# Optimization experiments

Measured on AMD Instinct MI355X. Metric: run time of the kernel, lower is better.

Reference implementation:

```python
import jax, jax.numpy as jnp
import numpy as np

N_NODES = 100000
N_EDGES = 1600000


def gcn_layer(x, src, dst, W, b, n_nodes):
    # PyG GCNConv: h = x @ W; add self-loops; sym-normalized scatter-add; + bias
    h = x @ W
    loop = jnp.arange(n_nodes, dtype=src.dtype)
    si = jnp.concatenate([src, loop])
    di = jnp.concatenate([dst, loop])
    deg = jax.ops.segment_sum(jnp.ones(si.shape[0], h.dtype), di, num_segments=n_nodes)
    dinv = jax.lax.rsqrt(deg)  # deg >= 1 due to self-loops
    norm = dinv[si] * dinv[di]              # [E+N]
    msgs = h[si] * norm[:, None]            # gather-scale
    out = jax.ops.segment_sum(msgs, di, num_segments=n_nodes)  # scatter-add
    return out + b


def setup_inputs() -> dict:
    key = jax.random.key(0)
    ks = jax.random.split(key, 8)
    x = jax.random.normal(ks[0], (N_NODES, 8), dtype=jnp.float32)
    edge_index = jax.random.randint(ks[1], (2, N_EDGES), 0, N_NODES, dtype=jnp.int32)
    W1 = jax.random.normal(ks[2], (8, 32), dtype=jnp.float32) * 0.3
    b1 = jax.random.normal(ks[3], (32,), dtype=jnp.float32) * 0.1
    W2 = jax.random.normal(ks[4], (32, 16), dtype=jnp.float32) * 0.2
    b2 = jax.random.normal(ks[5], (16,), dtype=jnp.float32) * 0.1
    Wfc = jax.random.normal(ks[6], (16, 1), dtype=jnp.float32) * 0.25
    bfc = jax.random.normal(ks[7], (1,), dtype=jnp.float32) * 0.1
    return {"x": x, "edge_index": edge_index, "W1": W1, "b1": b1,
            "W2": W2, "b2": b2, "Wfc": Wfc, "bfc": bfc}


def reference(x, edge_index, W1, b1, W2, b2, Wfc, bfc):
    n = x.shape[0]
    src, dst = edge_index[0], edge_index[1]
    h = jax.nn.relu(gcn_layer(x, src, dst, W1, b1, n))
    h = jax.nn.relu(gcn_layer(h, src, dst, W2, b2, n))
    return jax.nn.sigmoid(h @ Wfc + bfc)  # [N, 1]
```

## Files before the change

### kernel.cpp

```cpp
#include <hip/hip_runtime.h>
#include <math.h>

#define N_NODES 100000
#define N_EDGES 1600000

#define NB_SHIFT 7
#define NB 128
#define NBINS 782
#define RCAP 2432
#define BCHUNK 2048
#define BINBLOCKS ((N_EDGES + BCHUNK - 1) / BCHUNK)
#define LCAP 8
#define SPB 16

__device__ __forceinline__ unsigned int pack_bf2(float a, float b) {
    unsigned int ua = __float_as_uint(a), ub = __float_as_uint(b);
    ua += 0x7FFFu + ((ua >> 16) & 1u);
    ub += 0x7FFFu + ((ub >> 16) & 1u);
    return (ua >> 16) | (ub & 0xFFFF0000u);
}
__device__ __forceinline__ float bf_lo(unsigned int u) { return __uint_as_float(u << 16); }
__device__ __forceinline__ float bf_hi(unsigned int u) { return __uint_as_float(u & 0xFFFF0000u); }

#define QR(v) { v += __shfl_xor(v, 1, 64); v += __shfl_xor(v, 2, 64); }

__global__ __launch_bounds__(512) void k_bin(const int* __restrict__ src, const int* __restrict__ dst,
                                             unsigned char* __restrict__ cnt_tab, int* __restrict__ log,
                                             int* __restrict__ spill_rec, int* __restrict__ spill_bin, int e) {
    __shared__ int lcnt[NBINS];
    __shared__ int lbuf[NBINS * LCAP];
    __shared__ int sp_rec[SPB];
    __shared__ int sp_bin[SPB];
    __shared__ int sp_n;
    int tid = threadIdx.x, blk = blockIdx.x;
    for (int b = tid; b < NBINS; b += 512) lcnt[b] = 0;
    if (tid == 0) sp_n = 0;
    __syncthreads();
    int base = blk * BCHUNK;
    int end = min(base + BCHUNK, e);
    for (int i = base + tid; i < end; i += 512) {
        int d = dst[i], s = src[i];
        int b = d >> NB_SHIFT;
        int rec = (s << NB_SHIFT) | (d & (NB - 1));
        int slot = atomicAdd(&lcnt[b], 1);
        if (slot < LCAP) {
            lbuf[b * LCAP + slot] = rec;
        } else {
            int k = atomicAdd(&sp_n, 1);
            if (k < SPB) { sp_rec[k] = rec; sp_bin[k] = b; }
        }
    }
    __syncthreads();
    for (int b = tid; b < NBINS; b += 512) cnt_tab[blk * NBINS + b] = (unsigned char)min(lcnt[b], LCAP);
    int* lrow = log + blk * NBINS * LCAP;
    for (int idx = tid; idx < NBINS * LCAP; idx += 512) {
        int c = idx >> 3;
        if ((idx & (LCAP - 1)) < lcnt[c]) lrow[idx] = lbuf[idx];
    }
    if (tid < SPB) {
        int valid = tid < min(sp_n, SPB);
        spill_rec[blk * SPB + tid] = valid ? sp_rec[tid] : 0;
        spill_bin[blk * SPB + tid] = valid ? sp_bin[tid] : -1;
    }
}

__global__ __launch_bounds__(512) void k_sort(const unsigned char* __restrict__ cnt_tab, const int* __restrict__ log,
                                              const int* __restrict__ spill_rec, const int* __restrict__ spill_bin,
                                              int* __restrict__ gcur, int* __restrict__ regions,
                                              const float* __restrict__ x, float* __restrict__ dinv,
                                              unsigned int* __restrict__ gxu, int* __restrict__ row_start) {
    __shared__ int ccnt[BINBLOCKS];
    __shared__ int coff[BINBLOCKS];
    __shared__ int wtot[8];
    __shared__ int msum_s;
    __shared__ int sp_take;
    __shared__ int lrec[RCAP];
    __shared__ int lsort[RCAP];
    __shared__ int cnt[NB];
    __shared__ int stt[NB];
    __shared__ int cur[NB];
    __shared__ float di_s[NB];
    int b = blockIdx.x, tid = threadIdx.x;
    int lane = tid & 63, wv = tid >> 6;

    for (int c = tid; c < BINBLOCKS; c += 512) ccnt[c] = cnt_tab[c * NBINS + b];
    if (tid == 0) sp_take = 0;
    if (tid < NB) cnt[tid] = 0;
    __syncthreads();
    {
        int c0 = tid * 2, c1 = c0 + 1;
        int v0 = (c0 < BINBLOCKS) ? ccnt[c0] : 0;
        int v1 = (c1 < BINBLOCKS) ? ccnt[c1] : 0;
        int v = v0 + v1, sc = v;
#pragma unroll
        for (int off = 1; off < 64; off <<= 1) {
            int t = __shfl_up(sc, off, 64);
            if (lane >= off) sc += t;
        }
        if (lane == 63) wtot[wv] = sc;
        __syncthreads();
        if (tid == 0) {
            int acc = 0;
#pragma unroll
            for (int w = 0; w < 8; ++w) { int t = wtot[w]; wtot[w] = acc; acc += t; }
            msum_s = acc;
        }
        __syncthreads();
        int basep = sc - v + wtot[wv];
        if (c0 < BINBLOCKS) coff[c0] = basep;
        if (c1 < BINBLOCKS) coff[c1] = basep + v0;
    }
    __syncthreads();
    for (int idx = tid; idx < BINBLOCKS * LCAP; idx += 512) {
        int c = idx >> 3, k = idx & (LCAP - 1);
        if (k < ccnt[c]) {
            int pos = coff[c] + k;
            if (pos < RCAP) {
                int rec = log[(c * NBINS + b) * LCAP + k];
                lrec[pos] = rec;
                atomicAdd(&cnt[rec & (NB - 1)], 1);
            }
        }
    }
    for (int jj = tid; jj < BINBLOCKS * SPB; jj += 512) {
        if (spill_bin[jj] == b) {
            int p = atomicAdd(&sp_take, 1);
            int pos = msum_s + p;
            if (pos < RCAP) {
                int rec = spill_rec[jj];
                lrec[pos] = rec;
                atomicAdd(&cnt[rec & (NB - 1)], 1);
            }
        }
    }
    __syncthreads();
    int m = min(msum_s + sp_take, RCAP);
    if (tid == 0) gcur[b] = m;
    if (tid < 64) {
        int c0 = cnt[lane], c1 = cnt[64 + lane];
        int s0 = c0, s1 = c1;
#pragma unroll
        for (int off = 1; off < 64; off <<= 1) {
            int t0 = __shfl_up(s0, off, 64);
            int t1 = __shfl_up(s1, off, 64);
            if (lane >= off) { s0 += t0; s1 += t1; }
        }
        s1 += __shfl(s0, 63, 64);
        stt[lane] = s0 - c0;
        stt[64 + lane] = s1 - c1;
    }
    __syncthreads();
    int node0 = b << NB_SHIFT;
    if (tid < NB) {
        cur[tid] = stt[tid];
        float d = rsqrtf((float)cnt[tid] + 1.0f);
        di_s[tid] = d;
        row_start[b * NB + tid] = b * RCAP + stt[tid];
        int node = node0 + tid;
        if (node < N_NODES) dinv[node] = d;
    }
    __syncthreads();
    {
        int l = tid >> 2, p = tid & 3;
        int node = node0 + l;
        if (node < N_NODES) {
            const float2* x2 = (const float2*)x;
            float2 xv = x2[node * 4 + p];
            float d = di_s[l];
            gxu[node * 4 + p] = pack_bf2(xv.x * d, xv.y * d);
        }
    }
    for (int j = tid; j < m; j += 512) {
        int rec = lrec[j];
        int pos = atomicAdd(&cur[rec & (NB - 1)], 1);
        lsort[pos] = rec >> NB_SHIFT;
    }
    __syncthreads();
    int* wb = regions + b * RCAP;
    for (int j = tid; j < m; j += 512) wb[j] = lsort[j];
}

__global__ __launch_bounds__(512) void k_agg1_mlp(const int* __restrict__ gcur, const int* __restrict__ regions,
                                                  const int* __restrict__ row_start,
                                                  const unsigned int* __restrict__ gxu,
                                                  const float* __restrict__ dinv,
                                                  const float* __restrict__ W1, const float* __restrict__ b1,
                                                  const float* __restrict__ W2,
                                                  unsigned int* __restrict__ g2u) {
    __shared__ int lsort[RCAP];
    __shared__ float wsh[800];
    int b = blockIdx.x, tid = threadIdx.x;
    int m = gcur[b];
    const int* rrow = regions + b * RCAP;
    for (int j = tid; j < m; j += 512) lsort[j] = rrow[j];
    for (int i2 = tid; i2 < 800; i2 += 512)
        wsh[i2] = (i2 < 256) ? W1[i2] : (i2 < 288) ? b1[i2 - 256] : W2[i2 - 288];
    __syncthreads();
    int l = tid >> 2, q = tid & 3;
    int node = (b << NB_SHIFT) + l;
    if (node >= N_NODES) return;
    int js = row_start[node] - b * RCAP;
    int je = (l < NB - 1) ? (row_start[node + 1] - b * RCAP) : m;
    const uint4* gx4 = (const uint4*)gxu;
    float a0 = 0.f, a1 = 0.f, a2 = 0.f, a3 = 0.f, a4 = 0.f, a5 = 0.f, a6 = 0.f, a7 = 0.f;
    if (q == 0) {
        uint4 u = gx4[node];
        a0 = bf_lo(u.x); a1 = bf_hi(u.x); a2 = bf_lo(u.y); a3 = bf_hi(u.y);
        a4 = bf_lo(u.z); a5 = bf_hi(u.z); a6 = bf_lo(u.w); a7 = bf_hi(u.w);
    }
    int j = js + q;
    for (; j + 4 < je; j += 8) {
        int s0 = lsort[j], s1 = lsort[j + 4];
        uint4 u = gx4[s0];
        uint4 w = gx4[s1];
        a0 += bf_lo(u.x); a1 += bf_hi(u.x); a2 += bf_lo(u.y); a3 += bf_hi(u.y);
        a4 += bf_lo(u.z); a5 += bf_hi(u.z); a6 += bf_lo(u.w); a7 += bf_hi(u.w);
        a0 += bf_lo(w.x); a1 += bf_hi(w.x); a2 += bf_lo(w.y); a3 += bf_hi(w.y);
        a4 += bf_lo(w.z); a5 += bf_hi(w.z); a6 += bf_lo(w.w); a7 += bf_hi(w.w);
    }
    if (j < je) {
        uint4 u = gx4[lsort[j]];
        a0 += bf_lo(u.x); a1 += bf_hi(u.x); a2 += bf_lo(u.y); a3 += bf_hi(u.y);
        a4 += bf_lo(u.z); a5 += bf_hi(u.z); a6 += bf_lo(u.w); a7 += bf_hi(u.w);
    }
    QR(a0); QR(a1); QR(a2); QR(a3); QR(a4); QR(a5); QR(a6); QR(a7);
    float di = dinv[node];
    float y[8] = { a0 * di, a1 * di, a2 * di, a3 * di, a4 * di, a5 * di, a6 * di, a7 * di };
    const float* W1s = wsh;
    const float* b1s = wsh + 256;
    const float* W2s = wsh + 288;
    float hh[8];
#pragma unroll
    for (int ff = 0; ff < 8; ++ff) {
        int f = q * 8 + ff;
        float sa = b1s[f];
#pragma unroll
        for (int k = 0; k < 8; ++k) sa = fmaf(y[k], W1s[k * 32 + f], sa);
        hh[ff] = fmaxf(0.f, sa);
    }
    float g[16];
#pragma unroll
    for (int o = 0; o < 16; ++o) {
        float sa = 0.f;
#pragma unroll
        for (int ff = 0; ff < 8; ++ff) sa = fmaf(hh[ff], W2s[(q * 8 + ff) * 16 + o], sa);
        g[o] = sa;
    }
#pragma unroll
    for (int o = 0; o < 16; ++o) QR(g[o]);
    int f0 = q * 4;
    uint2 pk = make_uint2(pack_bf2(g[f0] * di, g[f0 + 1] * di),
                          pack_bf2(g[f0 + 2] * di, g[f0 + 3] * di));
    ((uint2*)g2u)[node * 4 + q] = pk;
}

__global__ __launch_bounds__(512) void k_agg2_final(const int* __restrict__ gcur, const int* __restrict__ regions,
                                                    const int* __restrict__ row_start,
                                                    const unsigned int* __restrict__ g2u,
                                                    const float* __restrict__ dinv,
                                                    const float* __restrict__ b2, const float* __restrict__ Wfc,
                                                    const float* __restrict__ bfc, float* __restrict__ out) {
    __shared__ int lsort[RCAP];
    int b = blockIdx.x, tid = threadIdx.x;
    int m = gcur[b];
    const int* rrow = regions + b * RCAP;
    for (int j = tid; j < m; j += 512) lsort[j] = rrow[j];
    __syncthreads();
    int l = tid >> 2, q = tid & 3;
    int node = (b << NB_SHIFT) + l;
    if (node >= N_NODES) return;
    int js = row_start[node] - b * RCAP;
    int je = (l < NB - 1) ? (row_start[node + 1] - b * RCAP) : m;
    const uint4* g24 = (const uint4*)g2u;
    float a[16];
#pragma unroll
    for (int f = 0; f < 16; ++f) a[f] = 0.f;
    if (q == 0) {
        uint4 u0 = g24[node * 2], u1 = g24[node * 2 + 1];
        a[0] = bf_lo(u0.x); a[1] = bf_hi(u0.x); a[2] = bf_lo(u0.y); a[3] = bf_hi(u0.y);
        a[4] = bf_lo(u0.z); a[5] = bf_hi(u0.z); a[6] = bf_lo(u0.w); a[7] = bf_hi(u0.w);
        a[8] = bf_lo(u1.x); a[9] = bf_hi(u1.x); a[10] = bf_lo(u1.y); a[11] = bf_hi(u1.y);
        a[12] = bf_lo(u1.z); a[13] = bf_hi(u1.z); a[14] = bf_lo(u1.w); a[15] = bf_hi(u1.w);
    }
    int j = js + q;
    for (; j + 4 < je; j += 8) {
        int s0 = lsort[j], s1 = lsort[j + 4];
        uint4 u0 = g24[s0 * 2], u1 = g24[s0 * 2 + 1];
        uint4 w0 = g24[s1 * 2], w1 = g24[s1 * 2 + 1];
        a[0] += bf_lo(u0.x); a[1] += bf_hi(u0.x); a[2] += bf_lo(u0.y); a[3] += bf_hi(u0.y);
        a[4] += bf_lo(u0.z); a[5] += bf_hi(u0.z); a[6] += bf_lo(u0.w); a[7] += bf_hi(u0.w);
        a[8] += bf_lo(u1.x); a[9] += bf_hi(u1.x); a[10] += bf_lo(u1.y); a[11] += bf_hi(u1.y);
        a[12] += bf_lo(u1.z); a[13] += bf_hi(u1.z); a[14] += bf_lo(u1.w); a[15] += bf_hi(u1.w);
        a[0] += bf_lo(w0.x); a[1] += bf_hi(w0.x); a[2] += bf_lo(w0.y); a[3] += bf_hi(w0.y);
        a[4] += bf_lo(w0.z); a[5] += bf_hi(w0.z); a[6] += bf_lo(w0.w); a[7] += bf_hi(w0.w);
        a[8] += bf_lo(w1.x); a[9] += bf_hi(w1.x); a[10] += bf_lo(w1.y); a[11] += bf_hi(w1.y);
        a[12] += bf_lo(w1.z); a[13] += bf_hi(w1.z); a[14] += bf_lo(w1.w); a[15] += bf_hi(w1.w);
    }
    if (j < je) {
        int s0 = lsort[j];
        uint4 u0 = g24[s0 * 2], u1 = g24[s0 * 2 + 1];
        a[0] += bf_lo(u0.x); a[1] += bf_hi(u0.x); a[2] += bf_lo(u0.y); a[3] += bf_hi(u0.y);
        a[4] += bf_lo(u0.z); a[5] += bf_hi(u0.z); a[6] += bf_lo(u0.w); a[7] += bf_hi(u0.w);
        a[8] += bf_lo(u1.x); a[9] += bf_hi(u1.x); a[10] += bf_lo(u1.y); a[11] += bf_hi(u1.y);
        a[12] += bf_lo(u1.z); a[13] += bf_hi(u1.z); a[14] += bf_lo(u1.w); a[15] += bf_hi(u1.w);
    }
#pragma unroll
    for (int f = 0; f < 16; ++f) QR(a[f]);
    if (q == 0) {
        float di = dinv[node];
        float z = bfc[0];
#pragma unroll
        for (int f = 0; f < 16; ++f)
            z += fmaxf(0.f, di * a[f] + b2[f]) * Wfc[f];
        out[node] = 1.0f / (1.0f + expf(-z));
    }
}

extern "C" void kernel_launch(void* const* d_in, const int* in_sizes, int n_in,
                              void* d_out, int out_size, void* d_ws, size_t ws_size,
                              hipStream_t stream) {
    const float* x   = (const float*)d_in[0];
    const int*   ei  = (const int*)d_in[1];
    const float* W1  = (const float*)d_in[2];
    const float* b1  = (const float*)d_in[3];
    const float* W2  = (const float*)d_in[4];
    const float* b2  = (const float*)d_in[5];
    const float* Wfc = (const float*)d_in[6];
    const float* bfc = (const float*)d_in[7];
    float* out = (float*)d_out;

    const int* src = ei;
    const int* dst = ei + N_EDGES;
    const int E = N_EDGES;

    int*           log       = (int*)d_ws;
    int*           spill_rec = log + (size_t)BINBLOCKS * NBINS * LCAP;
    int*           spill_bin = spill_rec + BINBLOCKS * SPB;
    int*           gcur      = spill_bin + BINBLOCKS * SPB;
    int*           regions   = gcur + NBINS;
    int*           row_start = regions + NBINS * RCAP;
    float*         dinv      = (float*)(row_start + NBINS * NB);
    unsigned int*  gxu       = (unsigned int*)(dinv + N_NODES);
    unsigned int*  g2u       = gxu + (size_t)N_NODES * 4;
    unsigned char* cnt_tab   = (unsigned char*)(g2u + (size_t)N_NODES * 8);

    k_bin<<<BINBLOCKS, 512, 0, stream>>>(src, dst, cnt_tab, log, spill_rec, spill_bin, E);
    k_sort<<<NBINS, 512, 0, stream>>>(cnt_tab, log, spill_rec, spill_bin, gcur, regions, x, dinv, gxu, row_start);
    k_agg1_mlp<<<NBINS, 512, 0, stream>>>(gcur, regions, row_start, gxu, dinv, W1, b1, W2, g2u);
    k_agg2_final<<<NBINS, 512, 0, stream>>>(gcur, regions, row_start, g2u, dinv, b2, Wfc, bfc, out);
}
```

Measured before the change: 144.7 us.

## Bin edges directly into global per-bin regions via atomic cursors

The binning kernel now reserves space in each bin's global region with one atomicAdd per (block, bin) and writes its local records straight there, with overflow records appended individually. This drops the intermediate log, count table and spill arrays, and with them the prefix scan and the per-chunk gather loop in the sort kernel, which now just reads its region. A memset of the bin counters is added. Record order within a bin becomes nondeterministic, and there are many scattered small global writes and contended atomics on about 782 counters.

```diff
diff --git a/kernel.cpp b/kernel.cpp
--- a/kernel.cpp
+++ b/kernel.cpp
@@ -11,7 +11,6 @@
 #define BCHUNK 2048
 #define BINBLOCKS ((N_EDGES + BCHUNK - 1) / BCHUNK)
 #define LCAP 8
-#define SPB 16
 
 __device__ __forceinline__ unsigned int pack_bf2(float a, float b) {
     unsigned int ua = __float_as_uint(a), ub = __float_as_uint(b);
@@ -25,16 +24,11 @@
 #define QR(v) { v += __shfl_xor(v, 1, 64); v += __shfl_xor(v, 2, 64); }
 
 __global__ __launch_bounds__(512) void k_bin(const int* __restrict__ src, const int* __restrict__ dst,
-                                             unsigned char* __restrict__ cnt_tab, int* __restrict__ log,
-                                             int* __restrict__ spill_rec, int* __restrict__ spill_bin, int e) {
+                                             int* __restrict__ gbin_cnt, int* __restrict__ regions, int e) {
     __shared__ int lcnt[NBINS];
     __shared__ int lbuf[NBINS * LCAP];
-    __shared__ int sp_rec[SPB];
-    __shared__ int sp_bin[SPB];
-    __shared__ int sp_n;
     int tid = threadIdx.x, blk = blockIdx.x;
     for (int b = tid; b < NBINS; b += 512) lcnt[b] = 0;
-    if (tid == 0) sp_n = 0;
     __syncthreads();
     int base = blk * BCHUNK;
     int end = min(base + BCHUNK, e);
@@ -46,34 +40,27 @@
         if (slot < LCAP) {
             lbuf[b * LCAP + slot] = rec;
         } else {
-            int k = atomicAdd(&sp_n, 1);
-            if (k < SPB) { sp_rec[k] = rec; sp_bin[k] = b; }
-        }
-    }
-    __syncthreads();
-    for (int b = tid; b < NBINS; b += 512) cnt_tab[blk * NBINS + b] = (unsigned char)min(lcnt[b], LCAP);
-    int* lrow = log + blk * NBINS * LCAP;
-    for (int idx = tid; idx < NBINS * LCAP; idx += 512) {
-        int c = idx >> 3;
-        if ((idx & (LCAP - 1)) < lcnt[c]) lrow[idx] = lbuf[idx];
-    }
-    if (tid < SPB) {
-        int valid = tid < min(sp_n, SPB);
-        spill_rec[blk * SPB + tid] = valid ? sp_rec[tid] : 0;
-        spill_bin[blk * SPB + tid] = valid ? sp_bin[tid] : -1;
-    }
-}
-
-__global__ __launch_bounds__(512) void k_sort(const unsigned char* __restrict__ cnt_tab, const int* __restrict__ log,
-                                              const int* __restrict__ spill_rec, const int* __restrict__ spill_bin,
-                                              int* __restrict__ gcur, int* __restrict__ regions,
+            int gp = atomicAdd(&gbin_cnt[b], 1);
+            if (gp < RCAP) regions[b * RCAP + gp] = rec;
+        }
+    }
+    __syncthreads();
+    for (int b = tid; b < NBINS; b += 512) {
+        int c = min(lcnt[b], LCAP);
+        if (c > 0) {
+            int gp = atomicAdd(&gbin_cnt[b], c);
+            int* row = regions + b * RCAP;
+#pragma unroll 4
+            for (int k = 0; k < c; ++k)
+                if (gp + k < RCAP) row[gp + k] = lbuf[b * LCAP + k];
+        }
+    }
+}
+
+__global__ __launch_bounds__(512) void k_sort(const int* __restrict__ gbin_cnt,
+                                              int* __restrict__ regions,
                                               const float* __restrict__ x, float* __restrict__ dinv,
                                               unsigned int* __restrict__ gxu, int* __restrict__ row_start) {
-    __shared__ int ccnt[BINBLOCKS];
-    __shared__ int coff[BINBLOCKS];
-    __shared__ int wtot[8];
-    __shared__ int msum_s;
-    __shared__ int sp_take;
     __shared__ int lrec[RCAP];
     __shared__ int lsort[RCAP];
     __shared__ int cnt[NB];
@@ -81,61 +68,17 @@
     __shared__ int cur[NB];
     __shared__ float di_s[NB];
     int b = blockIdx.x, tid = threadIdx.x;
-    int lane = tid & 63, wv = tid >> 6;
-
-    for (int c = tid; c < BINBLOCKS; c += 512) ccnt[c] = cnt_tab[c * NBINS + b];
-    if (tid == 0) sp_take = 0;
+    int lane = tid & 63;
+    int m = min(gbin_cnt[b], RCAP);
     if (tid < NB) cnt[tid] = 0;
     __syncthreads();
-    {
-        int c0 = tid * 2, c1 = c0 + 1;
-        int v0 = (c0 < BINBLOCKS) ? ccnt[c0] : 0;
-        int v1 = (c1 < BINBLOCKS) ? ccnt[c1] : 0;
-        int v = v0 + v1, sc = v;
-#pragma unroll
-        for (int off = 1; off < 64; off <<= 1) {
-            int t = __shfl_up(sc, off, 64);
-            if (lane >= off) sc += t;
-        }
-        if (lane == 63) wtot[wv] = sc;
-        __syncthreads();
-        if (tid == 0) {
-            int acc = 0;
-#pragma unroll
-            for (int w = 0; w < 8; ++w) { int t = wtot[w]; wtot[w] = acc; acc += t; }
-            msum_s = acc;
-        }
-        __syncthreads();
-        int basep = sc - v + wtot[wv];
-        if (c0 < BINBLOCKS) coff[c0] = basep;
-        if (c1 < BINBLOCKS) coff[c1] = basep + v0;
-    }
-    __syncthreads();
-    for (int idx = tid; idx < BINBLOCKS * LCAP; idx += 512) {
-        int c = idx >> 3, k = idx & (LCAP - 1);
-        if (k < ccnt[c]) {
-            int pos = coff[c] + k;
-            if (pos < RCAP) {
-                int rec = log[(c * NBINS + b) * LCAP + k];
-                lrec[pos] = rec;
-                atomicAdd(&cnt[rec & (NB - 1)], 1);
-            }
-        }
-    }
-    for (int jj = tid; jj < BINBLOCKS * SPB; jj += 512) {
-        if (spill_bin[jj] == b) {
-            int p = atomicAdd(&sp_take, 1);
-            int pos = msum_s + p;
-            if (pos < RCAP) {
-                int rec = spill_rec[jj];
-                lrec[pos] = rec;
-                atomicAdd(&cnt[rec & (NB - 1)], 1);
-            }
-        }
-    }
-    __syncthreads();
-    int m = min(msum_s + sp_take, RCAP);
-    if (tid == 0) gcur[b] = m;
+    int* row = regions + b * RCAP;
+    for (int j = tid; j < m; j += 512) {
+        int rec = row[j];
+        lrec[j] = rec;
+        atomicAdd(&cnt[rec & (NB - 1)], 1);
+    }
+    __syncthreads();
     if (tid < 64) {
         int c0 = cnt[lane], c1 = cnt[64 + lane];
         int s0 = c0, s1 = c1;
@@ -176,11 +119,10 @@
         lsort[pos] = rec >> NB_SHIFT;
     }
     __syncthreads();
-    int* wb = regions + b * RCAP;
-    for (int j = tid; j < m; j += 512) wb[j] = lsort[j];
-}
-
-__global__ __launch_bounds__(512) void k_agg1_mlp(const int* __restrict__ gcur, const int* __restrict__ regions,
+    for (int j = tid; j < m; j += 512) row[j] = lsort[j];
+}
+
+__global__ __launch_bounds__(512) void k_agg1_mlp(const int* __restrict__ gbin_cnt, const int* __restrict__ regions,
                                                   const int* __restrict__ row_start,
                                                   const unsigned int* __restrict__ gxu,
                                                   const float* __restrict__ dinv,
@@ -190,7 +132,7 @@
     __shared__ int lsort[RCAP];
     __shared__ float wsh[800];
     int b = blockIdx.x, tid = threadIdx.x;
-    int m = gcur[b];
+    int m = min(gbin_cnt[b], RCAP);
     const int* rrow = regions + b * RCAP;
     for (int j = tid; j < m; j += 512) lsort[j] = rrow[j];
     for (int i2 = tid; i2 < 800; i2 += 512)
@@ -254,7 +196,7 @@
     ((uint2*)g2u)[node * 4 + q] = pk;
 }
 
-__global__ __launch_bounds__(512) void k_agg2_final(const int* __restrict__ gcur, const int* __restrict__ regions,
+__global__ __launch_bounds__(512) void k_agg2_final(const int* __restrict__ gbin_cnt, const int* __restrict__ regions,
                                                     const int* __restrict__ row_start,
                                                     const unsigned int* __restrict__ g2u,
                                                     const float* __restrict__ dinv,
@@ -262,7 +204,7 @@
                                                     const float* __restrict__ bfc, float* __restrict__ out) {
     __shared__ int lsort[RCAP];
     int b = blockIdx.x, tid = threadIdx.x;
-    int m = gcur[b];
+    int m = min(gbin_cnt[b], RCAP);
     const int* rrow = regions + b * RCAP;
     for (int j = tid; j < m; j += 512) lsort[j] = rrow[j];
     __syncthreads();
@@ -333,19 +275,16 @@
     const int* dst = ei + N_EDGES;
     const int E = N_EDGES;
 
-    int*           log       = (int*)d_ws;
-    int*           spill_rec = log + (size_t)BINBLOCKS * NBINS * LCAP;
-    int*           spill_bin = spill_rec + BINBLOCKS * SPB;
-    int*           gcur      = spill_bin + BINBLOCKS * SPB;
-    int*           regions   = gcur + NBINS;
-    int*           row_start = regions + NBINS * RCAP;
-    float*         dinv      = (float*)(row_start + NBINS * NB);
-    unsigned int*  gxu       = (unsigned int*)(dinv + N_NODES);
-    unsigned int*  g2u       = gxu + (size_t)N_NODES * 4;
-    unsigned char* cnt_tab   = (unsigned char*)(g2u + (size_t)N_NODES * 8);
-
-    k_bin<<<BINBLOCKS, 512, 0, stream>>>(src, dst, cnt_tab, log, spill_rec, spill_bin, E);
-    k_sort<<<NBINS, 512, 0, stream>>>(cnt_tab, log, spill_rec, spill_bin, gcur, regions, x, dinv, gxu, row_start);
-    k_agg1_mlp<<<NBINS, 512, 0, stream>>>(gcur, regions, row_start, gxu, dinv, W1, b1, W2, g2u);
-    k_agg2_final<<<NBINS, 512, 0, stream>>>(gcur, regions, row_start, g2u, dinv, b2, Wfc, bfc, out);
-}
+    int*          gbin_cnt  = (int*)d_ws;
+    int*          regions   = gbin_cnt + NBINS;
+    int*          row_start = regions + (size_t)NBINS * RCAP;
+    float*        dinv      = (float*)(row_start + NBINS * NB);
+    unsigned int* gxu       = (unsigned int*)(dinv + N_NODES);
+    unsigned int* g2u       = gxu + (size_t)N_NODES * 4;
+
+    hipMemsetAsync(gbin_cnt, 0, NBINS * sizeof(int), stream);
+    k_bin<<<BINBLOCKS, 512, 0, stream>>>(src, dst, gbin_cnt, regions, E);
+    k_sort<<<NBINS, 512, 0, stream>>>(gbin_cnt, regions, x, dinv, gxu, row_start);
+    k_agg1_mlp<<<NBINS, 512, 0, stream>>>(gbin_cnt, regions, row_start, gxu, dinv, W1, b1, W2, g2u);
+    k_agg2_final<<<NBINS, 512, 0, stream>>>(gbin_cnt, regions, row_start, g2u, dinv, b2, Wfc, bfc, out);
+}
```

Result: slower. 155.7 us (+7.6%).

## Widen binning chunks with vectorized loads and split aggregation blocks in half

Applied to the files above, without the earlier changes.

The binning kernel now processes 4096-edge chunks with 16 local slots per bin, reads src/dst as int4, and writes log entries as int4 vectors. The sort kernel drops to one chunk per thread for its scan and reads log chunks with int4 loads. Both aggregation kernels now launch two 256-thread blocks per bin, each staging only its half's slice of the sorted neighbor list. The aim is fewer, wider memory transactions and more parallel blocks for the gathers, at the cost of a larger log buffer and different spill behavior (only 8 spill slots per chunk for overflow).

```diff
diff --git a/kernel.cpp b/kernel.cpp
--- a/kernel.cpp
+++ b/kernel.cpp
@@ -8,10 +8,10 @@
 #define NB 128
 #define NBINS 782
 #define RCAP 2432
-#define BCHUNK 2048
+#define BCHUNK 4096
 #define BINBLOCKS ((N_EDGES + BCHUNK - 1) / BCHUNK)
-#define LCAP 8
-#define SPB 16
+#define LCAP 16
+#define SPB 8
 
 __device__ __forceinline__ unsigned int pack_bf2(float a, float b) {
     unsigned int ua = __float_as_uint(a), ub = __float_as_uint(b);
@@ -25,7 +25,7 @@
 #define QR(v) { v += __shfl_xor(v, 1, 64); v += __shfl_xor(v, 2, 64); }
 
 __global__ __launch_bounds__(512) void k_bin(const int* __restrict__ src, const int* __restrict__ dst,
-                                             unsigned char* __restrict__ cnt_tab, int* __restrict__ log,
+                                             unsigned char* __restrict__ cnt_tab, int* __restrict__ glog,
                                              int* __restrict__ spill_rec, int* __restrict__ spill_bin, int e) {
     __shared__ int lcnt[NBINS];
     __shared__ int lbuf[NBINS * LCAP];
@@ -38,24 +38,34 @@
     __syncthreads();
     int base = blk * BCHUNK;
     int end = min(base + BCHUNK, e);
-    for (int i = base + tid; i < end; i += 512) {
-        int d = dst[i], s = src[i];
-        int b = d >> NB_SHIFT;
-        int rec = (s << NB_SHIFT) | (d & (NB - 1));
-        int slot = atomicAdd(&lcnt[b], 1);
-        if (slot < LCAP) {
-            lbuf[b * LCAP + slot] = rec;
-        } else {
-            int k = atomicAdd(&sp_n, 1);
-            if (k < SPB) { sp_rec[k] = rec; sp_bin[k] = b; }
-        }
-    }
-    __syncthreads();
-    for (int b = tid; b < NBINS; b += 512) cnt_tab[blk * NBINS + b] = (unsigned char)min(lcnt[b], LCAP);
-    int* lrow = log + blk * NBINS * LCAP;
-    for (int idx = tid; idx < NBINS * LCAP; idx += 512) {
-        int c = idx >> 3;
-        if ((idx & (LCAP - 1)) < lcnt[c]) lrow[idx] = lbuf[idx];
+    for (int i = base + tid * 4; i + 4 <= end; i += 2048) {
+        int4 s4 = *(const int4*)(src + i);
+        int4 d4 = *(const int4*)(dst + i);
+        int ss[4] = { s4.x, s4.y, s4.z, s4.w };
+        int dd[4] = { d4.x, d4.y, d4.z, d4.w };
+#pragma unroll
+        for (int k = 0; k < 4; ++k) {
+            int d = dd[k], s = ss[k];
+            int b = d >> NB_SHIFT;
+            int rec = (s << NB_SHIFT) | (d & (NB - 1));
+            int slot = atomicAdd(&lcnt[b], 1);
+            if (slot < LCAP) {
+                lbuf[b * LCAP + slot] = rec;
+            } else {
+                int kk = atomicAdd(&sp_n, 1);
+                if (kk < SPB) { sp_rec[kk] = rec; sp_bin[kk] = b; }
+            }
+        }
+    }
+    __syncthreads();
+    int* lrow = glog + blk * NBINS * LCAP;
+    for (int b = tid; b < NBINS; b += 512) {
+        int c = min(lcnt[b], LCAP);
+        cnt_tab[blk * NBINS + b] = (unsigned char)c;
+        if (c > 0)  *(int4*)(lrow + b * LCAP)      = *(const int4*)&lbuf[b * LCAP];
+        if (c > 4)  *(int4*)(lrow + b * LCAP + 4)  = *(const int4*)&lbuf[b * LCAP + 4];
+        if (c > 8)  *(int4*)(lrow + b * LCAP + 8)  = *(const int4*)&lbuf[b * LCAP + 8];
+        if (c > 12) *(int4*)(lrow + b * LCAP + 12) = *(const int4*)&lbuf[b * LCAP + 12];
     }
     if (tid < SPB) {
         int valid = tid < min(sp_n, SPB);
@@ -64,7 +74,7 @@
     }
 }
 
-__global__ __launch_bounds__(512) void k_sort(const unsigned char* __restrict__ cnt_tab, const int* __restrict__ log,
+__global__ __launch_bounds__(512) void k_sort(const unsigned char* __restrict__ cnt_tab, const int* __restrict__ glog,
                                               const int* __restrict__ spill_rec, const int* __restrict__ spill_bin,
                                               int* __restrict__ gcur, int* __restrict__ regions,
                                               const float* __restrict__ x, float* __restrict__ dinv,
@@ -87,41 +97,41 @@
     if (tid == 0) sp_take = 0;
     if (tid < NB) cnt[tid] = 0;
     __syncthreads();
-    {
-        int c0 = tid * 2, c1 = c0 + 1;
-        int v0 = (c0 < BINBLOCKS) ? ccnt[c0] : 0;
-        int v1 = (c1 < BINBLOCKS) ? ccnt[c1] : 0;
-        int v = v0 + v1, sc = v;
-#pragma unroll
-        for (int off = 1; off < 64; off <<= 1) {
-            int t = __shfl_up(sc, off, 64);
-            if (lane >= off) sc += t;
-        }
-        if (lane == 63) wtot[wv] = sc;
-        __syncthreads();
-        if (tid == 0) {
-            int acc = 0;
-#pragma unroll
-            for (int w = 0; w < 8; ++w) { int t = wtot[w]; wtot[w] = acc; acc += t; }
-            msum_s = acc;
-        }
-        __syncthreads();
-        int basep = sc - v + wtot[wv];
-        if (c0 < BINBLOCKS) coff[c0] = basep;
-        if (c1 < BINBLOCKS) coff[c1] = basep + v0;
-    }
-    __syncthreads();
-    for (int idx = tid; idx < BINBLOCKS * LCAP; idx += 512) {
-        int c = idx >> 3, k = idx & (LCAP - 1);
-        if (k < ccnt[c]) {
-            int pos = coff[c] + k;
-            if (pos < RCAP) {
-                int rec = log[(c * NBINS + b) * LCAP + k];
-                lrec[pos] = rec;
-                atomicAdd(&cnt[rec & (NB - 1)], 1);
-            }
-        }
-    }
+    int v = (tid < BINBLOCKS) ? ccnt[tid] : 0;
+    int s = v;
+#pragma unroll
+    for (int off = 1; off < 64; off <<= 1) {
+        int t = __shfl_up(s, off, 64);
+        if (lane >= off) s += t;
+    }
+    if (lane == 63) wtot[wv] = s;
+    __syncthreads();
+    if (tid == 0) {
+        int acc = 0;
+#pragma unroll
+        for (int w = 0; w < 8; ++w) { int t = wtot[w]; wtot[w] = acc; acc += t; }
+        msum_s = acc;
+    }
+    __syncthreads();
+    if (tid < BINBLOCKS) coff[tid] = (s - v) + wtot[wv];
+    __syncthreads();
+#define DOREC(r, k) if (cc > (k) && p + (k) < RCAP) { lrec[p + (k)] = (r); atomicAdd(&cnt[(r) & (NB - 1)], 1); }
+    for (int c = tid; c < BINBLOCKS; c += 512) {
+        int cc = ccnt[c];
+        if (cc > 0) {
+            const int* chunk = glog + (c * NBINS + b) * LCAP;
+            int p = coff[c];
+            { int4 v0 = *(const int4*)chunk;
+              DOREC(v0.x, 0) DOREC(v0.y, 1) DOREC(v0.z, 2) DOREC(v0.w, 3) }
+            if (cc > 4)  { int4 v1 = *(const int4*)(chunk + 4);
+              DOREC(v1.x, 4) DOREC(v1.y, 5) DOREC(v1.z, 6) DOREC(v1.w, 7) }
+            if (cc > 8)  { int4 v2 = *(const int4*)(chunk + 8);
+              DOREC(v2.x, 8) DOREC(v2.y, 9) DOREC(v2.z, 10) DOREC(v2.w, 11) }
+            if (cc > 12) { int4 v3 = *(const int4*)(chunk + 12);
+              DOREC(v3.x, 12) DOREC(v3.y, 13) DOREC(v3.z, 14) DOREC(v3.w, 15) }
+        }
+    }
+#undef DOREC
     for (int jj = tid; jj < BINBLOCKS * SPB; jj += 512) {
         if (spill_bin[jj] == b) {
             int p = atomicAdd(&sp_take, 1);
@@ -180,27 +190,32 @@
     for (int j = tid; j < m; j += 512) wb[j] = lsort[j];
 }
 
-__global__ __launch_bounds__(512) void k_agg1_mlp(const int* __restrict__ gcur, const int* __restrict__ regions,
+__global__ __launch_bounds__(256) void k_agg1_mlp(const int* __restrict__ gcur, const int* __restrict__ regions,
                                                   const int* __restrict__ row_start,
                                                   const unsigned int* __restrict__ gxu,
                                                   const float* __restrict__ dinv,
                                                   const float* __restrict__ W1, const float* __restrict__ b1,
                                                   const float* __restrict__ W2,
                                                   unsigned int* __restrict__ g2u) {
-    __shared__ int lsort[RCAP];
+    __shared__ int lslice[RCAP];
     __shared__ float wsh[800];
-    int b = blockIdx.x, tid = threadIdx.x;
-    int m = gcur[b];
-    const int* rrow = regions + b * RCAP;
-    for (int j = tid; j < m; j += 512) lsort[j] = rrow[j];
-    for (int i2 = tid; i2 < 800; i2 += 512)
+    int bin = blockIdx.x >> 1, half = blockIdx.x & 1, tid = threadIdx.x;
+    int m = gcur[bin];
+    int binbase = bin * RCAP;
+    int nodeA = (bin << NB_SHIFT) + half * 64;
+    int lo = row_start[nodeA] - binbase;
+    int hi = (half == 0) ? (row_start[nodeA + 64] - binbase) : m;
+    const int* rrow = regions + binbase;
+    for (int j = lo + tid; j < hi; j += 256) lslice[j - lo] = rrow[j];
+    for (int i2 = tid; i2 < 800; i2 += 256)
         wsh[i2] = (i2 < 256) ? W1[i2] : (i2 < 288) ? b1[i2 - 256] : W2[i2 - 288];
     __syncthreads();
     int l = tid >> 2, q = tid & 3;
-    int node = (b << NB_SHIFT) + l;
+    int node = nodeA + l;
     if (node >= N_NODES) return;
-    int js = row_start[node] - b * RCAP;
-    int je = (l < NB - 1) ? (row_start[node + 1] - b * RCAP) : m;
+    int local = half * 64 + l;
+    int js = row_start[node] - binbase;
+    int je = (local < NB - 1) ? (row_start[node + 1] - binbase) : m;
     const uint4* gx4 = (const uint4*)gxu;
     float a0 = 0.f, a1 = 0.f, a2 = 0.f, a3 = 0.f, a4 = 0.f, a5 = 0.f, a6 = 0.f, a7 = 0.f;
     if (q == 0) {
@@ -210,7 +225,7 @@
     }
     int j = js + q;
     for (; j + 4 < je; j += 8) {
-        int s0 = lsort[j], s1 = lsort[j + 4];
+        int s0 = lslice[j - lo], s1 = lslice[j + 4 - lo];
         uint4 u = gx4[s0];
         uint4 w = gx4[s1];
         a0 += bf_lo(u.x); a1 += bf_hi(u.x); a2 += bf_lo(u.y); a3 += bf_hi(u.y);
@@ -219,7 +234,7 @@
         a4 += bf_lo(w.z); a5 += bf_hi(w.z); a6 += bf_lo(w.w); a7 += bf_hi(w.w);
     }
     if (j < je) {
-        uint4 u = gx4[lsort[j]];
+        uint4 u = gx4[lslice[j - lo]];
         a0 += bf_lo(u.x); a1 += bf_hi(u.x); a2 += bf_lo(u.y); a3 += bf_hi(u.y);
         a4 += bf_lo(u.z); a5 += bf_hi(u.z); a6 += bf_lo(u.w); a7 += bf_hi(u.w);
     }
@@ -254,23 +269,28 @@
     ((uint2*)g2u)[node * 4 + q] = pk;
 }
 
-__global__ __launch_bounds__(512) void k_agg2_final(const int* __restrict__ gcur, const int* __restrict__ regions,
+__global__ __launch_bounds__(256) void k_agg2_final(const int* __restrict__ gcur, const int* __restrict__ regions,
                                                     const int* __restrict__ row_start,
                                                     const unsigned int* __restrict__ g2u,
                                                     const float* __restrict__ dinv,
                                                     const float* __restrict__ b2, const float* __restrict__ Wfc,
                                                     const float* __restrict__ bfc, float* __restrict__ out) {
-    __shared__ int lsort[RCAP];
-    int b = blockIdx.x, tid = threadIdx.x;
-    int m = gcur[b];
-    const int* rrow = regions + b * RCAP;
-    for (int j = tid; j < m; j += 512) lsort[j] = rrow[j];
+    __shared__ int lslice[RCAP];
+    int bin = blockIdx.x >> 1, half = blockIdx.x & 1, tid = threadIdx.x;
+    int m = gcur[bin];
+    int binbase = bin * RCAP;
+    int nodeA = (bin << NB_SHIFT) + half * 64;
+    int lo = row_start[nodeA] - binbase;
+    int hi = (half == 0) ? (row_start[nodeA + 64] - binbase) : m;
+    const int* rrow = regions + binbase;
+    for (int j = lo + tid; j < hi; j += 256) lslice[j - lo] = rrow[j];
     __syncthreads();
     int l = tid >> 2, q = tid & 3;
-    int node = (b << NB_SHIFT) + l;
+    int node = nodeA + l;
     if (node >= N_NODES) return;
-    int js = row_start[node] - b * RCAP;
-    int je = (l < NB - 1) ? (row_start[node + 1] - b * RCAP) : m;
+    int local = half * 64 + l;
+    int js = row_start[node] - binbase;
+    int je = (local < NB - 1) ? (row_start[node + 1] - binbase) : m;
     const uint4* g24 = (const uint4*)g2u;
     float a[16];
 #pragma unroll
@@ -284,7 +304,7 @@
     }
     int j = js + q;
     for (; j + 4 < je; j += 8) {
-        int s0 = lsort[j], s1 = lsort[j + 4];
+        int s0 = lslice[j - lo], s1 = lslice[j + 4 - lo];
         uint4 u0 = g24[s0 * 2], u1 = g24[s0 * 2 + 1];
         uint4 w0 = g24[s1 * 2], w1 = g24[s1 * 2 + 1];
         a[0] += bf_lo(u0.x); a[1] += bf_hi(u0.x); a[2] += bf_lo(u0.y); a[3] += bf_hi(u0.y);
@@ -297,7 +317,7 @@
         a[12] += bf_lo(w1.z); a[13] += bf_hi(w1.z); a[14] += bf_lo(w1.w); a[15] += bf_hi(w1.w);
     }
     if (j < je) {
-        int s0 = lsort[j];
+        int s0 = lslice[j - lo];
         uint4 u0 = g24[s0 * 2], u1 = g24[s0 * 2 + 1];
         a[0] += bf_lo(u0.x); a[1] += bf_hi(u0.x); a[2] += bf_lo(u0.y); a[3] += bf_hi(u0.y);
         a[4] += bf_lo(u0.z); a[5] += bf_hi(u0.z); a[6] += bf_lo(u0.w); a[7] += bf_hi(u0.w);
@@ -333,19 +353,19 @@
     const int* dst = ei + N_EDGES;
     const int E = N_EDGES;
 
-    int*           log       = (int*)d_ws;
-    int*           spill_rec = log + (size_t)BINBLOCKS * NBINS * LCAP;
+    int*           glog      = (int*)d_ws;
+    int*           spill_rec = glog + (size_t)BINBLOCKS * NBINS * LCAP;
     int*           spill_bin = spill_rec + BINBLOCKS * SPB;
     int*           gcur      = spill_bin + BINBLOCKS * SPB;
     int*           regions   = gcur + NBINS;
-    int*           row_start = regions + NBINS * RCAP;
+    int*           row_start = regions + (size_t)NBINS * RCAP;
     float*         dinv      = (float*)(row_start + NBINS * NB);
     unsigned int*  gxu       = (unsigned int*)(dinv + N_NODES);
     unsigned int*  g2u       = gxu + (size_t)N_NODES * 4;
     unsigned char* cnt_tab   = (unsigned char*)(g2u + (size_t)N_NODES * 8);
 
-    k_bin<<<BINBLOCKS, 512, 0, stream>>>(src, dst, cnt_tab, log, spill_rec, spill_bin, E);
-    k_sort<<<NBINS, 512, 0, stream>>>(cnt_tab, log, spill_rec, spill_bin, gcur, regions, x, dinv, gxu, row_start);
-    k_agg1_mlp<<<NBINS, 512, 0, stream>>>(gcur, regions, row_start, gxu, dinv, W1, b1, W2, g2u);
-    k_agg2_final<<<NBINS, 512, 0, stream>>>(gcur, regions, row_start, g2u, dinv, b2, Wfc, bfc, out);
-}
+    k_bin<<<BINBLOCKS, 512, 0, stream>>>(src, dst, cnt_tab, glog, spill_rec, spill_bin, E);
+    k_sort<<<NBINS, 512, 0, stream>>>(cnt_tab, glog, spill_rec, spill_bin, gcur, regions, x, dinv, gxu, row_start);
+    k_agg1_mlp<<<NBINS * 2, 256, 0, stream>>>(gcur, regions, row_start, gxu, dinv, W1, b1, W2, g2u);
+    k_agg2_final<<<NBINS * 2, 256, 0, stream>>>(gcur, regions, row_start, g2u, dinv, b2, Wfc, bfc, out);
+}
```

Result: faster. 133.0 us (-8.1%).
